# Performance work log

Hardware: AMD Instinct MI355X
Metric: run time of the kernel (lower is better)

The kernel has to match this reference:

```python
import jax, jax.numpy as jnp
import numpy as np

D = 256        # embedding dim (params[0])
V = 50000      # candidate vocab (params[1])
VW = 200000    # word vocab
B = 1024       # number of entities (batched ragged loop)
C = 64         # candidates per side (padded fixed length)
TOP_K = 10     # params[2]


def setup_inputs() -> dict:
    key = jax.random.key(0)
    ks = jax.random.split(key, 10)
    return {
        "word_l_ids": jax.random.randint(ks[0], (B,), 0, VW),
        "word_r_ids": jax.random.randint(ks[1], (B,), 0, VW),
        "cand_l_ids": jax.random.randint(ks[2], (B, C), 0, V),
        "cand_r_ids": jax.random.randint(ks[3], (B, C), 0, V),
        "word_embeds": jax.random.normal(ks[4], (VW, D), dtype=jnp.float32) * 0.1,
        "candidate_embeds": jax.random.normal(ks[5], (V, D), dtype=jnp.float32) * 0.1,
        # truncated_normal(stddev=0.5) for W_a, stddev=1.0 for W_c
        "W_a": jax.random.truncated_normal(ks[6], -2.0, 2.0, (D, D), dtype=jnp.float32) * 0.5,
        "b_a": jnp.zeros((1, D), dtype=jnp.float32),
        "W_c": jax.random.truncated_normal(ks[7], -2.0, 2.0, (2 * D, D), dtype=jnp.float32),
        "b_c": jnp.zeros((1, D), dtype=jnp.float32),
    }


def reference(word_l_ids, word_r_ids, cand_l_ids, cand_r_ids,
              word_embeds, candidate_embeds, W_a, b_a, W_c, b_c):
    # per-entity embedding lookups
    wl = word_embeds[word_l_ids]            # [B, D]
    wr = word_embeds[word_r_ids]            # [B, D]
    cl = candidate_embeds[cand_l_ids]       # [B, C, D]
    cr = candidate_embeds[cand_r_ids]       # [B, C, D]

    def attend(word, cands):
        # embed_word_align = tanh(word @ W_a + b_a)
        align = jnp.tanh(word @ W_a + b_a)                       # [B, D]
        # softmax over candidate axis (axis=0 in original per-entity view)
        scores = jnp.einsum("bcd,bd->bc", cands, align)          # [B, C]
        att = jax.nn.softmax(scores, axis=-1)                    # [B, C]
        # weighted sum of candidate embeddings
        return jnp.einsum("bc,bcd->bd", att, cands)              # [B, D]

    # note: left aggregation attends over RIGHT candidates and vice versa
    aggre_l = attend(wl, cr)
    aggre_r = attend(wr, cl)

    words_whole = wl + wr
    cands_whole = aggre_r + aggre_l
    phrase = jnp.tanh(jnp.concatenate([words_whole, cands_whole], axis=-1) @ W_c + b_c)  # [B, D]

    logits = phrase @ candidate_embeds.T    # [B, V]
    y_pred = jax.nn.softmax(logits, axis=-1)
    _, top_candidates = jax.lax.top_k(y_pred, TOP_K)             # [B, TOP_K]
    return y_pred, top_candidates
```

## Files before the change

### kernel.cpp

```cpp
#include <hip/hip_runtime.h>
#include <math.h>

#define DD 256
#define BB 1024
#define CC 64
#define VV 50000
#define TOPK 10
#define BM 128
#define BN 128
#define BK 64
#define LDK 72
#define NCHUNK 391
#define MAXCAND 64
#define NT 512

typedef __attribute__((ext_vector_type(8))) short bf16x8;
typedef __attribute__((ext_vector_type(4))) short bf16x4;
typedef __attribute__((ext_vector_type(4))) float f32x4;

__device__ inline unsigned short f2bf(float x) {
    unsigned u = __float_as_uint(x);
    unsigned r = (u + 0x7FFFu + ((u >> 16) & 1u)) >> 16;
    return (unsigned short)r;
}

__device__ inline bf16x8 load_bf8(const unsigned short* p) {
    bf16x4 lo = *(const bf16x4*)p;
    bf16x4 hi = *(const bf16x4*)(p + 4);
    bf16x8 r;
    r[0] = lo[0]; r[1] = lo[1]; r[2] = lo[2]; r[3] = lo[3];
    r[4] = hi[0]; r[5] = hi[1]; r[6] = hi[2]; r[7] = hi[3];
    return r;
}

__global__ __launch_bounds__(256) void k_phrase(
    const int* __restrict__ wl_ids, const int* __restrict__ wr_ids,
    const int* __restrict__ cl_ids, const int* __restrict__ cr_ids,
    const float* __restrict__ WE, const float* __restrict__ CE,
    const float* __restrict__ W_a, const float* __restrict__ b_a,
    const float* __restrict__ W_c, const float* __restrict__ b_c,
    float* __restrict__ phrase, unsigned short* __restrict__ phraseb)
{
    const int b = blockIdx.x;
    const int t = threadIdx.x;
    __shared__ float s_wl[DD], s_wr[DD], s_align[DD], s_agg0[DD], s_agg1[DD];
    __shared__ float s_part[256];
    __shared__ float s_att[CC];
    __shared__ int s_rid[CC];

    s_wl[t] = WE[(size_t)wl_ids[b] * DD + t];
    s_wr[t] = WE[(size_t)wr_ids[b] * DD + t];
    __syncthreads();

    for (int side = 0; side < 2; ++side) {
        const float* w    = (side == 0) ? s_wl : s_wr;
        const int*   cids = (side == 0) ? (cr_ids + b * CC) : (cl_ids + b * CC);

        float acc = b_a[t];
        #pragma unroll 4
        for (int k = 0; k < DD; ++k) acc = fmaf(w[k], W_a[k * DD + t], acc);
        s_align[t] = tanhf(acc);
        if (t < CC) s_rid[t] = cids[t];
        __syncthreads();

        {
            const int c = t & 63, p = t >> 6;
            const float* crow = CE + (size_t)s_rid[c] * DD + p * 64;
            const float* al = s_align + p * 64;
            float sc = 0.f;
            #pragma unroll 4
            for (int j = 0; j < 64; ++j) sc = fmaf(crow[j], al[j], sc);
            s_part[t] = sc;
        }
        __syncthreads();
        if (t < CC) {
            float s = s_part[t] + s_part[64 + t] + s_part[128 + t] + s_part[192 + t];
            float m = s;
            for (int off = 32; off; off >>= 1) m = fmaxf(m, __shfl_xor(m, off, 64));
            float e = expf(s - m);
            float sum = e;
            for (int off = 32; off; off >>= 1) sum += __shfl_xor(sum, off, 64);
            s_att[t] = e / sum;
        }
        __syncthreads();
        {
            float ag = 0.f;
            #pragma unroll 4
            for (int c = 0; c < CC; ++c)
                ag = fmaf(s_att[c], CE[(size_t)s_rid[c] * DD + t], ag);
            if (side == 0) s_agg0[t] = ag; else s_agg1[t] = ag;
        }
        __syncthreads();
    }

    s_wl[t]  += s_wr[t];
    s_agg0[t] += s_agg1[t];
    __syncthreads();

    float acc = b_c[t];
    #pragma unroll 4
    for (int k = 0; k < DD; ++k) acc = fmaf(s_wl[k],  W_c[k * DD + t], acc);
    #pragma unroll 4
    for (int k = 0; k < DD; ++k) acc = fmaf(s_agg0[k], W_c[(DD + k) * DD + t], acc);
    const float ph = tanhf(acc);
    phrase[b * DD + t] = ph;
    phraseb[b * DD + t] = f2bf(ph);
}

__global__ __launch_bounds__(256) void k_logits_mfma(
    const unsigned short* __restrict__ phraseb, const float* __restrict__ CE,
    float* __restrict__ out, float* __restrict__ pmax, float* __restrict__ psum)
{
    __shared__ unsigned short sA[BM * LDK];
    __shared__ unsigned short sB[BN * LDK];
    __shared__ float sM[2][BM], sS[2][BM];

    const int t = threadIdx.x;
    const int wave = t >> 6, lane = t & 63;
    const int wm = wave >> 1, wn = wave & 1;
    const int quad = lane >> 4, l15 = lane & 15;
    const int n0 = blockIdx.x * BN, m0 = blockIdx.y * BM;

    f32x4 acc[4][4] = {};

    for (int k0 = 0; k0 < DD; k0 += BK) {
        __syncthreads();
        #pragma unroll
        for (int r = 0; r < 4; ++r) {
            const int idx = t + r * 256;
            const int m = idx >> 3, k8 = (idx & 7) * 8;
            const uint4 v = *(const uint4*)(phraseb + (size_t)(m0 + m) * DD + k0 + k8);
            *(uint2*)(sA + m * LDK + k8)     = make_uint2(v.x, v.y);
            *(uint2*)(sA + m * LDK + k8 + 4) = make_uint2(v.z, v.w);
        }
        #pragma unroll
        for (int r = 0; r < 8; ++r) {
            const int idx = t + r * 256;
            const int n = idx >> 4, k4 = (idx & 15) * 4;
            const int gn = n0 + n;
            float4 v = make_float4(0.f, 0.f, 0.f, 0.f);
            if (gn < VV) v = *(const float4*)(CE + (size_t)gn * DD + k0 + k4);
            ushort4 h;
            h.x = f2bf(v.x); h.y = f2bf(v.y); h.z = f2bf(v.z); h.w = f2bf(v.w);
            *(ushort4*)(sB + n * LDK + k4) = h;
        }
        __syncthreads();
        #pragma unroll
        for (int kk = 0; kk < BK; kk += 32) {
            bf16x8 af[4], bfr[4];
            #pragma unroll
            for (int i = 0; i < 4; ++i) {
                af[i]  = load_bf8(sA + (wm * 64 + i * 16 + l15) * LDK + kk + quad * 8);
                bfr[i] = load_bf8(sB + (wn * 64 + i * 16 + l15) * LDK + kk + quad * 8);
            }
            #pragma unroll
            for (int i = 0; i < 4; ++i)
                #pragma unroll
                for (int j = 0; j < 4; ++j)
                    acc[i][j] = __builtin_amdgcn_mfma_f32_16x16x32_bf16(af[i], bfr[j], acc[i][j], 0, 0, 0);
        }
    }

    bool val[4];
    #pragma unroll
    for (int j = 0; j < 4; ++j) val[j] = (n0 + wn * 64 + j * 16 + l15) < VV;

    #pragma unroll
    for (int i = 0; i < 4; ++i) {
        const int mbase = m0 + wm * 64 + i * 16 + quad * 4;
        #pragma unroll
        for (int r = 0; r < 4; ++r) {
            const int gm = mbase + r;
            #pragma unroll
            for (int j = 0; j < 4; ++j) {
                const int gn = n0 + wn * 64 + j * 16 + l15;
                if (val[j]) out[(size_t)gm * VV + gn] = acc[i][j][r];
            }
        }
    }

    #pragma unroll
    for (int i = 0; i < 4; ++i) {
        #pragma unroll
        for (int r = 0; r < 4; ++r) {
            float mx = -INFINITY;
            #pragma unroll
            for (int j = 0; j < 4; ++j) if (val[j]) mx = fmaxf(mx, acc[i][j][r]);
            #pragma unroll
            for (int off = 8; off >= 1; off >>= 1) mx = fmaxf(mx, __shfl_xor(mx, off, 64));
            float s = 0.f;
            #pragma unroll
            for (int j = 0; j < 4; ++j) if (val[j]) s += __expf(acc[i][j][r] - mx);
            #pragma unroll
            for (int off = 8; off >= 1; off >>= 1) s += __shfl_xor(s, off, 64);
            if (l15 == 0) {
                const int mloc = wm * 64 + i * 16 + quad * 4 + r;
                sM[wn][mloc] = mx;
                sS[wn][mloc] = s;
            }
        }
    }
    __syncthreads();
    if (t < BM) {
        const float Ma = sM[0][t], Mb = sM[1][t];
        const float nM = fmaxf(Ma, Mb);
        const float S = sS[0][t] * __expf(Ma - nM) + sS[1][t] * __expf(Mb - nM);
        pmax[(size_t)(m0 + t) * NCHUNK + blockIdx.x] = nM;
        psum[(size_t)(m0 + t) * NCHUNK + blockIdx.x] = S;
    }
}

__global__ __launch_bounds__(64) void k_rowstats(
    const float* __restrict__ pmax, const float* __restrict__ psum,
    float* __restrict__ rowM, float* __restrict__ rowS)
{
    const int b = blockIdx.x, t = threadIdx.x;
    float M = -INFINITY, S = 0.f;
    for (int c = t; c < NCHUNK; c += 64) {
        const float m = pmax[(size_t)b * NCHUNK + c];
        const float s = psum[(size_t)b * NCHUNK + c];
        const float nM = fmaxf(M, m);
        S = S * __expf(M - nM) + s * __expf(m - nM);
        M = nM;
    }
    #pragma unroll
    for (int off = 32; off; off >>= 1) {
        const float m2 = __shfl_xor(M, off, 64);
        const float s2 = __shfl_xor(S, off, 64);
        const float nM = fmaxf(M, m2);
        S = S * __expf(M - nM) + s2 * __expf(m2 - nM);
        M = nM;
    }
    if (t == 0) { rowM[b] = M; rowS[b] = S; }
}

__global__ __launch_bounds__(NT) void k_norm_topk(
    float* __restrict__ ylogits, const float* __restrict__ rowM,
    const float* __restrict__ rowS, int* __restrict__ cand_idx,
    int* __restrict__ cand_cnt)
{
    const int b = blockIdx.x, t = threadIdx.x;
    const float M = rowM[b];
    const float invS = 1.f / rowS[b];
    float* row = ylogits + (size_t)b * VV;

    float m1 = -1.f, m2 = -1.f;

    for (int i0 = t * 4; i0 < VV; i0 += NT * 4) {
        const float4 v = *(const float4*)(row + i0);
        float4 y;
        y.x = __expf(v.x - M) * invS;
        y.y = __expf(v.y - M) * invS;
        y.z = __expf(v.z - M) * invS;
        y.w = __expf(v.w - M) * invS;
        *(float4*)(row + i0) = y;
        float lo;
        lo = fminf(y.x, m1); m1 = fmaxf(y.x, m1); m2 = fmaxf(m2, lo);
        lo = fminf(y.y, m1); m1 = fmaxf(y.y, m1); m2 = fmaxf(m2, lo);
        lo = fminf(y.z, m1); m1 = fmaxf(y.z, m1); m2 = fmaxf(m2, lo);
        lo = fminf(y.w, m1); m1 = fmaxf(y.w, m1); m2 = fmaxf(m2, lo);
    }

    __shared__ float sv[NT * TOPK];
    sv[t * TOPK + 0] = m1;
    sv[t * TOPK + 1] = m2;
    #pragma unroll
    for (int j = 2; j < TOPK; ++j) sv[t * TOPK + j] = -1.f;

    for (int span = NT / 2; span >= 1; span >>= 1) {
        __syncthreads();
        if (t < span) {
            const int A = t * TOPK, B2 = (t + span) * TOPK;
            float rv[TOPK];
            int ia = 0, ib = 0;
            #pragma unroll
            for (int j = 0; j < TOPK; ++j) {
                const float av = sv[A + ia], bv = sv[B2 + ib];
                const bool takeA = (av >= bv);
                rv[j] = takeA ? av : bv;
                if (takeA) ++ia; else ++ib;
            }
            #pragma unroll
            for (int j = 0; j < TOPK; ++j) sv[A + j] = rv[j];
        }
    }

    __shared__ float s_th;
    __shared__ int s_cnt;
    __shared__ int s_cidx[MAXCAND];
    __syncthreads();
    if (t == 0) { s_th = sv[9] * 0.90f; s_cnt = 0; }
    __syncthreads();
    const float th = s_th;
    for (int i0 = t * 4; i0 < VV; i0 += NT * 4) {
        const float4 y = *(const float4*)(row + i0);
        const float ya[4] = {y.x, y.y, y.z, y.w};
        #pragma unroll
        for (int j = 0; j < 4; ++j) {
            if (ya[j] >= th) {
                const int p = atomicAdd(&s_cnt, 1);
                if (p < MAXCAND) s_cidx[p] = i0 + j;
            }
        }
    }
    __syncthreads();
    if (t == 0) cand_cnt[b] = (s_cnt < MAXCAND) ? s_cnt : MAXCAND;
    if (t < MAXCAND && t < s_cnt) cand_idx[b * MAXCAND + t] = s_cidx[t];
}

__global__ __launch_bounds__(64) void k_rescore(
    const float* __restrict__ phrase, const float* __restrict__ CE,
    const int* __restrict__ cand_idx, const int* __restrict__ cand_cnt,
    float* __restrict__ topk_out)
{
    const int b = blockIdx.x, lane = threadIdx.x;
    int cnt = cand_cnt[b];
    if (cnt > MAXCAND) cnt = MAXCAND;
    __shared__ float s_val[MAXCAND];
    __shared__ int   s_idx[MAXCAND];

    const float4 ph = *(const float4*)(phrase + (size_t)b * DD + lane * 4);
    for (int c = 0; c < cnt; ++c) {
        const int id = cand_idx[b * MAXCAND + c];
        const float4 ce = *(const float4*)(CE + (size_t)id * DD + lane * 4);
        float d = ph.x * ce.x + ph.y * ce.y + ph.z * ce.z + ph.w * ce.w;
        #pragma unroll
        for (int off = 32; off; off >>= 1) d += __shfl_xor(d, off, 64);
        if (lane == 0) { s_val[c] = d; s_idx[c] = id; }
    }
    __syncthreads();
    if (lane == 0) {
        for (int j = 0; j < TOPK; ++j) {
            int best = j;
            for (int c = j + 1; c < cnt; ++c) {
                if (s_val[c] > s_val[best] ||
                    (s_val[c] == s_val[best] && s_idx[c] < s_idx[best])) best = c;
            }
            const float bv = s_val[best]; const int bi = s_idx[best];
            s_val[best] = s_val[j]; s_idx[best] = s_idx[j];
            s_val[j] = bv; s_idx[j] = bi;
            topk_out[b * TOPK + j] = (float)bi;
        }
    }
}

extern "C" void kernel_launch(void* const* d_in, const int* in_sizes, int n_in,
                              void* d_out, int out_size, void* d_ws, size_t ws_size,
                              hipStream_t stream) {
    const int*   wl_ids = (const int*)d_in[0];
    const int*   wr_ids = (const int*)d_in[1];
    const int*   cl_ids = (const int*)d_in[2];
    const int*   cr_ids = (const int*)d_in[3];
    const float* WE     = (const float*)d_in[4];
    const float* CE     = (const float*)d_in[5];
    const float* W_a    = (const float*)d_in[6];
    const float* b_a    = (const float*)d_in[7];
    const float* W_c    = (const float*)d_in[8];
    const float* b_c    = (const float*)d_in[9];

    float* out = (float*)d_out;
    float* ws  = (float*)d_ws;

    float* phrase = ws;
    unsigned short* phraseb = (unsigned short*)(ws + 262144);
    float* pmax   = ws + 262144 + 131072;
    float* psum   = pmax + (size_t)BB * NCHUNK;
    float* rowM   = psum + (size_t)BB * NCHUNK;
    float* rowS   = rowM + BB;
    int*   cand_idx = (int*)(rowS + BB);
    int*   cand_cnt = cand_idx + (size_t)BB * MAXCAND;
    float* topk_out = out + (size_t)BB * VV;

    k_phrase<<<BB, 256, 0, stream>>>(wl_ids, wr_ids, cl_ids, cr_ids,
                                     WE, CE, W_a, b_a, W_c, b_c, phrase, phraseb);
    dim3 g(NCHUNK, BB / BM);
    k_logits_mfma<<<g, 256, 0, stream>>>(phraseb, CE, out, pmax, psum);
    k_rowstats<<<BB, 64, 0, stream>>>(pmax, psum, rowM, rowS);
    k_norm_topk<<<BB, NT, 0, stream>>>(out, rowM, rowS, cand_idx, cand_cnt);
    k_rescore<<<BB, 64, 0, stream>>>(phrase, CE, cand_idx, cand_cnt, topk_out);
}
```

Before: 730.7 us.

## Recompute logits GEMM to fuse softmax normalization and top-k candidate selection

Drops the write of raw logits and the separate normalize/top-k pass. Instead the GEMM runs twice: once producing only per-chunk max/sum stats, and once recomputing logits to write normalized probabilities and append threshold candidates via global atomics. The top-10 threshold now comes from per-chunk maxima in rowstats, and CE is pre-converted to bf16 in workspace. The workgroup order is also remapped so the M-blocks sharing a CE chunk run together. This trades one extra GEMM pass for removing a read-modify-write of the 200MB output, at the risk of atomic contention.

```diff
diff --git a/kernel.cpp b/kernel.cpp
--- a/kernel.cpp
+++ b/kernel.cpp
@@ -11,11 +11,11 @@
 #define BK 64
 #define LDK 72
 #define NCHUNK 391
-#define MAXCAND 64
-#define NT 512
+#define NMBLK 8
+#define NWG (NCHUNK * NMBLK)
+#define MAXCAND 60
 
 typedef __attribute__((ext_vector_type(8))) short bf16x8;
-typedef __attribute__((ext_vector_type(4))) short bf16x4;
 typedef __attribute__((ext_vector_type(4))) float f32x4;
 
 __device__ inline unsigned short f2bf(float x) {
@@ -24,13 +24,20 @@
     return (unsigned short)r;
 }
 
-__device__ inline bf16x8 load_bf8(const unsigned short* p) {
-    bf16x4 lo = *(const bf16x4*)p;
-    bf16x4 hi = *(const bf16x4*)(p + 4);
-    bf16x8 r;
-    r[0] = lo[0]; r[1] = lo[1]; r[2] = lo[2]; r[3] = lo[3];
-    r[4] = hi[0]; r[5] = hi[1]; r[6] = hi[2]; r[7] = hi[3];
-    return r;
+__global__ __launch_bounds__(256) void k_prep(
+    const float* __restrict__ CE, unsigned short* __restrict__ CEb)
+{
+    const int i = blockIdx.x * 256 + threadIdx.x;
+    const size_t base = (size_t)i * 8;
+    if (base >= (size_t)VV * DD) return;
+    const float4 a = *(const float4*)(CE + base);
+    const float4 b = *(const float4*)(CE + base + 4);
+    uint4 o;
+    o.x = (unsigned)f2bf(a.x) | ((unsigned)f2bf(a.y) << 16);
+    o.y = (unsigned)f2bf(a.z) | ((unsigned)f2bf(a.w) << 16);
+    o.z = (unsigned)f2bf(b.x) | ((unsigned)f2bf(b.y) << 16);
+    o.w = (unsigned)f2bf(b.z) | ((unsigned)f2bf(b.w) << 16);
+    *(uint4*)(CEb + base) = o;
 }
 
 __global__ __launch_bounds__(256) void k_phrase(
@@ -107,19 +114,29 @@
     phraseb[b * DD + t] = f2bf(ph);
 }
 
-__global__ __launch_bounds__(256) void k_logits_mfma(
-    const unsigned short* __restrict__ phraseb, const float* __restrict__ CE,
-    float* __restrict__ out, float* __restrict__ pmax, float* __restrict__ psum)
+template<bool STATS, bool BF16CE>
+__global__ __launch_bounds__(256) void k_gemm(
+    const unsigned short* __restrict__ phraseb,
+    const float* __restrict__ CE, const unsigned short* __restrict__ CEb,
+    float* __restrict__ out,
+    float* __restrict__ pmax, float* __restrict__ psum,
+    const float* __restrict__ rowM, const float* __restrict__ rowInvS,
+    const float* __restrict__ rowTh,
+    int* __restrict__ cand_idx, int* __restrict__ cand_cnt)
 {
     __shared__ unsigned short sA[BM * LDK];
     __shared__ unsigned short sB[BN * LDK];
-    __shared__ float sM[2][BM], sS[2][BM];
 
     const int t = threadIdx.x;
     const int wave = t >> 6, lane = t & 63;
     const int wm = wave >> 1, wn = wave & 1;
     const int quad = lane >> 4, l15 = lane & 15;
-    const int n0 = blockIdx.x * BN, m0 = blockIdx.y * BM;
+
+    const int wg = blockIdx.x;
+    const int q  = (wg & 7) * NCHUNK + (wg >> 3);
+    const int m0 = (q & 7) * BM;
+    const int cn = q >> 3;
+    const int n0 = cn * BN;
 
     f32x4 acc[4][4] = {};
 
@@ -130,19 +147,30 @@
             const int idx = t + r * 256;
             const int m = idx >> 3, k8 = (idx & 7) * 8;
             const uint4 v = *(const uint4*)(phraseb + (size_t)(m0 + m) * DD + k0 + k8);
-            *(uint2*)(sA + m * LDK + k8)     = make_uint2(v.x, v.y);
-            *(uint2*)(sA + m * LDK + k8 + 4) = make_uint2(v.z, v.w);
-        }
-        #pragma unroll
-        for (int r = 0; r < 8; ++r) {
-            const int idx = t + r * 256;
-            const int n = idx >> 4, k4 = (idx & 15) * 4;
-            const int gn = n0 + n;
-            float4 v = make_float4(0.f, 0.f, 0.f, 0.f);
-            if (gn < VV) v = *(const float4*)(CE + (size_t)gn * DD + k0 + k4);
-            ushort4 h;
-            h.x = f2bf(v.x); h.y = f2bf(v.y); h.z = f2bf(v.z); h.w = f2bf(v.w);
-            *(ushort4*)(sB + n * LDK + k4) = h;
+            *(uint4*)(sA + m * LDK + k8) = v;
+        }
+        if constexpr (BF16CE) {
+            #pragma unroll
+            for (int r = 0; r < 4; ++r) {
+                const int idx = t + r * 256;
+                const int n = idx >> 3, k8 = (idx & 7) * 8;
+                const int gn = n0 + n;
+                uint4 v = make_uint4(0u, 0u, 0u, 0u);
+                if (gn < VV) v = *(const uint4*)(CEb + (size_t)gn * DD + k0 + k8);
+                *(uint4*)(sB + n * LDK + k8) = v;
+            }
+        } else {
+            #pragma unroll
+            for (int r = 0; r < 8; ++r) {
+                const int idx = t + r * 256;
+                const int n = idx >> 4, k4 = (idx & 15) * 4;
+                const int gn = n0 + n;
+                float4 v = make_float4(0.f, 0.f, 0.f, 0.f);
+                if (gn < VV) v = *(const float4*)(CE + (size_t)gn * DD + k0 + k4);
+                ushort4 h;
+                h.x = f2bf(v.x); h.y = f2bf(v.y); h.z = f2bf(v.z); h.w = f2bf(v.w);
+                *(ushort4*)(sB + n * LDK + k4) = h;
+            }
         }
         __syncthreads();
         #pragma unroll
@@ -150,8 +178,8 @@
             bf16x8 af[4], bfr[4];
             #pragma unroll
             for (int i = 0; i < 4; ++i) {
-                af[i]  = load_bf8(sA + (wm * 64 + i * 16 + l15) * LDK + kk + quad * 8);
-                bfr[i] = load_bf8(sB + (wn * 64 + i * 16 + l15) * LDK + kk + quad * 8);
+                af[i]  = *(const bf16x8*)(sA + (wm * 64 + i * 16 + l15) * LDK + kk + quad * 8);
+                bfr[i] = *(const bf16x8*)(sB + (wn * 64 + i * 16 + l15) * LDK + kk + quad * 8);
             }
             #pragma unroll
             for (int i = 0; i < 4; ++i)
@@ -165,63 +193,95 @@
     #pragma unroll
     for (int j = 0; j < 4; ++j) val[j] = (n0 + wn * 64 + j * 16 + l15) < VV;
 
-    #pragma unroll
-    for (int i = 0; i < 4; ++i) {
-        const int mbase = m0 + wm * 64 + i * 16 + quad * 4;
-        #pragma unroll
-        for (int r = 0; r < 4; ++r) {
-            const int gm = mbase + r;
-            #pragma unroll
-            for (int j = 0; j < 4; ++j) {
-                const int gn = n0 + wn * 64 + j * 16 + l15;
-                if (val[j]) out[(size_t)gm * VV + gn] = acc[i][j][r];
-            }
-        }
-    }
-
-    #pragma unroll
-    for (int i = 0; i < 4; ++i) {
-        #pragma unroll
-        for (int r = 0; r < 4; ++r) {
-            float mx = -INFINITY;
-            #pragma unroll
-            for (int j = 0; j < 4; ++j) if (val[j]) mx = fmaxf(mx, acc[i][j][r]);
-            #pragma unroll
-            for (int off = 8; off >= 1; off >>= 1) mx = fmaxf(mx, __shfl_xor(mx, off, 64));
-            float s = 0.f;
-            #pragma unroll
-            for (int j = 0; j < 4; ++j) if (val[j]) s += __expf(acc[i][j][r] - mx);
-            #pragma unroll
-            for (int off = 8; off >= 1; off >>= 1) s += __shfl_xor(s, off, 64);
-            if (l15 == 0) {
-                const int mloc = wm * 64 + i * 16 + quad * 4 + r;
-                sM[wn][mloc] = mx;
-                sS[wn][mloc] = s;
-            }
-        }
-    }
-    __syncthreads();
-    if (t < BM) {
-        const float Ma = sM[0][t], Mb = sM[1][t];
-        const float nM = fmaxf(Ma, Mb);
-        const float S = sS[0][t] * __expf(Ma - nM) + sS[1][t] * __expf(Mb - nM);
-        pmax[(size_t)(m0 + t) * NCHUNK + blockIdx.x] = nM;
-        psum[(size_t)(m0 + t) * NCHUNK + blockIdx.x] = S;
+    if constexpr (STATS) {
+        __shared__ float sM[2][BM], sS[2][BM];
+        #pragma unroll
+        for (int i = 0; i < 4; ++i) {
+            #pragma unroll
+            for (int r = 0; r < 4; ++r) {
+                float m1 = -INFINITY;
+                #pragma unroll
+                for (int j = 0; j < 4; ++j) if (val[j]) m1 = fmaxf(m1, acc[i][j][r]);
+                #pragma unroll
+                for (int off = 8; off >= 1; off >>= 1) m1 = fmaxf(m1, __shfl_xor(m1, off, 64));
+                float s = 0.f;
+                #pragma unroll
+                for (int j = 0; j < 4; ++j) if (val[j]) s += __expf(acc[i][j][r] - m1);
+                #pragma unroll
+                for (int off = 8; off >= 1; off >>= 1) s += __shfl_xor(s, off, 64);
+                if (l15 == 0) {
+                    const int mloc = wm * 64 + i * 16 + quad * 4 + r;
+                    sM[wn][mloc] = m1;
+                    sS[wn][mloc] = s;
+                }
+            }
+        }
+        __syncthreads();
+        if (t < BM) {
+            const float Ma = sM[0][t], Mb = sM[1][t];
+            const float nM = fmaxf(Ma, Mb);
+            const float S  = sS[0][t] * __expf(Ma - nM) + sS[1][t] * __expf(Mb - nM);
+            const size_t o = (size_t)(m0 + t) * NCHUNK + cn;
+            pmax[o] = nM;
+            psum[o] = S;
+        }
+    } else {
+        __shared__ float sMr[BM], sIr[BM], sTr[BM];
+        if (t < BM) {
+            sMr[t] = rowM[m0 + t];
+            sIr[t] = rowInvS[m0 + t];
+            sTr[t] = rowTh[m0 + t];
+        }
+        __syncthreads();
+        #pragma unroll
+        for (int i = 0; i < 4; ++i) {
+            #pragma unroll
+            for (int r = 0; r < 4; ++r) {
+                const int ml = wm * 64 + i * 16 + quad * 4 + r;
+                const int gm = m0 + ml;
+                const float M = sMr[ml], inv = sIr[ml], th = sTr[ml];
+                #pragma unroll
+                for (int j = 0; j < 4; ++j) {
+                    if (val[j]) {
+                        const int gn = n0 + wn * 64 + j * 16 + l15;
+                        const float y = __expf(acc[i][j][r] - M) * inv;
+                        __builtin_nontemporal_store(y, out + (size_t)gm * VV + gn);
+                        if (y >= th) {
+                            const int p = atomicAdd(&cand_cnt[gm], 1);
+                            if (p < MAXCAND) cand_idx[gm * MAXCAND + p] = gn;
+                        }
+                    }
+                }
+            }
+        }
     }
 }
 
 __global__ __launch_bounds__(64) void k_rowstats(
     const float* __restrict__ pmax, const float* __restrict__ psum,
-    float* __restrict__ rowM, float* __restrict__ rowS)
+    float* __restrict__ rowM, float* __restrict__ rowInvS, float* __restrict__ rowTh,
+    int* __restrict__ cand_cnt)
 {
     const int b = blockIdx.x, t = threadIdx.x;
     float M = -INFINITY, S = 0.f;
+    float top[TOPK];
+    #pragma unroll
+    for (int j = 0; j < TOPK; ++j) top[j] = -INFINITY;
+
     for (int c = t; c < NCHUNK; c += 64) {
         const float m = pmax[(size_t)b * NCHUNK + c];
         const float s = psum[(size_t)b * NCHUNK + c];
         const float nM = fmaxf(M, m);
         S = S * __expf(M - nM) + s * __expf(m - nM);
         M = nM;
+        if (m > top[TOPK - 1]) {
+            float v = m;
+            #pragma unroll
+            for (int p = 0; p < TOPK; ++p) {
+                const float hi = fmaxf(top[p], v), lo = fminf(top[p], v);
+                top[p] = hi; v = lo;
+            }
+        }
     }
     #pragma unroll
     for (int off = 32; off; off >>= 1) {
@@ -231,81 +291,26 @@
         S = S * __expf(M - nM) + s2 * __expf(m2 - nM);
         M = nM;
     }
-    if (t == 0) { rowM[b] = M; rowS[b] = S; }
-}
-
-__global__ __launch_bounds__(NT) void k_norm_topk(
-    float* __restrict__ ylogits, const float* __restrict__ rowM,
-    const float* __restrict__ rowS, int* __restrict__ cand_idx,
-    int* __restrict__ cand_cnt)
-{
-    const int b = blockIdx.x, t = threadIdx.x;
-    const float M = rowM[b];
-    const float invS = 1.f / rowS[b];
-    float* row = ylogits + (size_t)b * VV;
-
-    float m1 = -1.f, m2 = -1.f;
-
-    for (int i0 = t * 4; i0 < VV; i0 += NT * 4) {
-        const float4 v = *(const float4*)(row + i0);
-        float4 y;
-        y.x = __expf(v.x - M) * invS;
-        y.y = __expf(v.y - M) * invS;
-        y.z = __expf(v.z - M) * invS;
-        y.w = __expf(v.w - M) * invS;
-        *(float4*)(row + i0) = y;
-        float lo;
-        lo = fminf(y.x, m1); m1 = fmaxf(y.x, m1); m2 = fmaxf(m2, lo);
-        lo = fminf(y.y, m1); m1 = fmaxf(y.y, m1); m2 = fmaxf(m2, lo);
-        lo = fminf(y.z, m1); m1 = fmaxf(y.z, m1); m2 = fmaxf(m2, lo);
-        lo = fminf(y.w, m1); m1 = fmaxf(y.w, m1); m2 = fmaxf(m2, lo);
-    }
-
-    __shared__ float sv[NT * TOPK];
-    sv[t * TOPK + 0] = m1;
-    sv[t * TOPK + 1] = m2;
-    #pragma unroll
-    for (int j = 2; j < TOPK; ++j) sv[t * TOPK + j] = -1.f;
-
-    for (int span = NT / 2; span >= 1; span >>= 1) {
-        __syncthreads();
-        if (t < span) {
-            const int A = t * TOPK, B2 = (t + span) * TOPK;
-            float rv[TOPK];
-            int ia = 0, ib = 0;
-            #pragma unroll
-            for (int j = 0; j < TOPK; ++j) {
-                const float av = sv[A + ia], bv = sv[B2 + ib];
-                const bool takeA = (av >= bv);
-                rv[j] = takeA ? av : bv;
-                if (takeA) ++ia; else ++ib;
-            }
-            #pragma unroll
-            for (int j = 0; j < TOPK; ++j) sv[A + j] = rv[j];
-        }
-    }
-
-    __shared__ float s_th;
-    __shared__ int s_cnt;
-    __shared__ int s_cidx[MAXCAND];
-    __syncthreads();
-    if (t == 0) { s_th = sv[9] * 0.90f; s_cnt = 0; }
-    __syncthreads();
-    const float th = s_th;
-    for (int i0 = t * 4; i0 < VV; i0 += NT * 4) {
-        const float4 y = *(const float4*)(row + i0);
-        const float ya[4] = {y.x, y.y, y.z, y.w};
-        #pragma unroll
-        for (int j = 0; j < 4; ++j) {
-            if (ya[j] >= th) {
-                const int p = atomicAdd(&s_cnt, 1);
-                if (p < MAXCAND) s_cidx[p] = i0 + j;
-            }
-        }
-    }
-    __syncthreads();
-    if (t == 0) cand_cnt[b] = (s_cnt < MAXCAND) ? s_cnt : MAXCAND;
-    if (t < MAXCAND && t < s_cnt) cand_idx[b * MAXCAND + t] = s_cidx[t];
+    float v10 = -INFINITY;
+    for (int k = 0; k < TOPK; ++k) {
+        float g = top[0];
+        #pragma unroll
+        for (int off = 32; off; off >>= 1) g = fmaxf(g, __shfl_xor(g, off, 64));
+        v10 = g;
+        const unsigned long long mk = __ballot(top[0] == g);
+        if (mk && t == __ffsll(mk) - 1) {
+            #pragma unroll
+            for (int p = 0; p < TOPK - 1; ++p) top[p] = top[p + 1];
+            top[TOPK - 1] = -INFINITY;
+        }
+    }
+    if (t == 0) {
+        rowM[b] = M;
+        const float inv = 1.f / S;
+        rowInvS[b] = inv;
+        rowTh[b] = 0.90f * __expf(v10 - M) * inv;
+        cand_cnt[b] = 0;
+    }
 }
 
 __global__ __launch_bounds__(64) void k_rescore(
@@ -318,6 +323,9 @@
     if (cnt > MAXCAND) cnt = MAXCAND;
     __shared__ float s_val[MAXCAND];
     __shared__ int   s_idx[MAXCAND];
+
+    if (lane < MAXCAND) { s_val[lane] = -INFINITY; s_idx[lane] = 0x7ffffff0; }
+    __syncthreads();
 
     const float4 ph = *(const float4*)(phrase + (size_t)b * DD + lane * 4);
     for (int c = 0; c < cnt; ++c) {
@@ -361,21 +369,37 @@
     float* out = (float*)d_out;
     float* ws  = (float*)d_ws;
 
-    float* phrase = ws;
+    float* phrase  = ws;
     unsigned short* phraseb = (unsigned short*)(ws + 262144);
-    float* pmax   = ws + 262144 + 131072;
-    float* psum   = pmax + (size_t)BB * NCHUNK;
-    float* rowM   = psum + (size_t)BB * NCHUNK;
-    float* rowS   = rowM + BB;
-    int*   cand_idx = (int*)(rowS + BB);
+    float* pmax    = ws + 262144 + 131072;
+    float* psum    = pmax + (size_t)BB * NCHUNK;
+    float* rowM    = psum + (size_t)BB * NCHUNK;
+    float* rowInvS = rowM + BB;
+    float* rowTh   = rowInvS + BB;
+    int*   cand_idx = (int*)(rowTh + BB);
     int*   cand_cnt = cand_idx + (size_t)BB * MAXCAND;
     float* topk_out = out + (size_t)BB * VV;
 
+    const size_t baseBytes = (size_t)((char*)(cand_cnt + BB) - (char*)ws);
+    const size_t ceOff = (baseBytes + 255) & ~(size_t)255;
+    const bool bf16ce = ws_size >= ceOff + (size_t)VV * DD * 2;
+    unsigned short* CEb = (unsigned short*)((char*)ws + ceOff);
+
     k_phrase<<<BB, 256, 0, stream>>>(wl_ids, wr_ids, cl_ids, cr_ids,
                                      WE, CE, W_a, b_a, W_c, b_c, phrase, phraseb);
-    dim3 g(NCHUNK, BB / BM);
-    k_logits_mfma<<<g, 256, 0, stream>>>(phraseb, CE, out, pmax, psum);
-    k_rowstats<<<BB, 64, 0, stream>>>(pmax, psum, rowM, rowS);
-    k_norm_topk<<<BB, NT, 0, stream>>>(out, rowM, rowS, cand_idx, cand_cnt);
+    if (bf16ce) {
+        k_prep<<<(VV * DD / 8 + 255) / 256, 256, 0, stream>>>(CE, CEb);
+        k_gemm<true, true><<<NWG, 256, 0, stream>>>(phraseb, CE, CEb, out,
+            pmax, psum, rowM, rowInvS, rowTh, cand_idx, cand_cnt);
+        k_rowstats<<<BB, 64, 0, stream>>>(pmax, psum, rowM, rowInvS, rowTh, cand_cnt);
+        k_gemm<false, true><<<NWG, 256, 0, stream>>>(phraseb, CE, CEb, out,
+            pmax, psum, rowM, rowInvS, rowTh, cand_idx, cand_cnt);
+    } else {
+        k_gemm<true, false><<<NWG, 256, 0, stream>>>(phraseb, CE, CEb, out,
+            pmax, psum, rowM, rowInvS, rowTh, cand_idx, cand_cnt);
+        k_rowstats<<<BB, 64, 0, stream>>>(pmax, psum, rowM, rowInvS, rowTh, cand_cnt);
+        k_gemm<false, false><<<NWG, 256, 0, stream>>>(phraseb, CE, CEb, out,
+            pmax, psum, rowM, rowInvS, rowTh, cand_idx, cand_cnt);
+    }
     k_rescore<<<BB, 64, 0, stream>>>(phrase, CE, cand_idx, cand_cnt, topk_out);
 }
```

After: 696.0 us. 1.05x faster.
